# Performance work log

Hardware: AMD Instinct MI355X
Metric: run time of the kernel (lower is better)

Reference implementation:

```python
import jax, jax.numpy as jnp
import numpy as np

ENS, N_UNITS, N_HID, IN_DIM, OUT_DIM, BATCH = 10, 256, 7, 6, 201, 16384


def setup_inputs() -> dict:
    key = jax.random.key(0)
    ks = jax.random.split(key, 8)
    # He/fan-in scaled weights so activations stay sane through 8 ReLU layers
    W0 = jax.random.normal(ks[0], (ENS, IN_DIM, N_UNITS), jnp.float32) / np.sqrt(IN_DIM)
    b0 = jax.random.normal(ks[1], (ENS, N_UNITS), jnp.float32) * 0.01
    Wh = jax.random.normal(ks[2], (N_HID, ENS, N_UNITS, N_UNITS), jnp.float32) / np.sqrt(N_UNITS)
    bh = jax.random.normal(ks[3], (N_HID, ENS, N_UNITS), jnp.float32) * 0.01
    Wf = jax.random.normal(ks[4], (ENS, N_UNITS, OUT_DIM), jnp.float32) / np.sqrt(N_UNITS)
    bf = jax.random.normal(ks[5], (ENS, OUT_DIM), jnp.float32) * 0.01
    x = jax.random.normal(ks[6], (BATCH, IN_DIM), jnp.float32)
    return {"x": x, "W0": W0, "b0": b0, "Wh": Wh, "bh": bh, "Wf": Wf, "bf": bf}


def reference(x, W0, b0, Wh, bh, Wf, bf):
    # Ensemble of MLPs (grouped 1x1 conv == per-ensemble dense layers).
    # Input is broadcast to every ensemble member (torch.cat tiling).
    h = jax.nn.relu(jnp.einsum('bi,eio->beo', x, W0) + b0)  # (B, ens, 256)

    def step(h, wb):
        W, b = wb
        return jax.nn.relu(jnp.einsum('beh,eho->beo', h, W) + b), None

    h, _ = jax.lax.scan(step, h, (Wh, bh))  # 7 hidden layers
    y = jnp.einsum('beh,eho->beo', h, Wf) + bf  # (B, ens, out_dim), ens-major channels
    B, E, O = y.shape
    # Faithful to torch: view(B, out_dim, ens_size) on ens-major flat channels,
    # then mean over last dim (mixes strided channel chunks, not true ensemble mean).
    return y.reshape(B, O, E).mean(axis=-1)  # (B, out_dim)
```

## Files before the change

kernel.cpp:

```cpp
#include <hip/hip_runtime.h>

typedef unsigned int u32;
typedef unsigned short ushort_t;

typedef __attribute__((ext_vector_type(8)))  short bf16x8;
typedef __attribute__((ext_vector_type(16))) float f32x16;

#define ENS 10
#define NU 256
#define NHID 7
#define IN_DIM 6
#define OUT_DIM 201
#define BATCH 16384


#define WH_PER 65536
#define WH_TOT (NHID * ENS * WH_PER)
#define W0_PER 4096
#define W0_TOT (ENS * W0_PER)
#define WF_PER 57344
#define WF_TOT (ENS * WF_PER)
#define X_TOT ((BATCH / 32) * 64 * 8)

#define O_WHH 0
#define O_WHL (O_WHH + WH_TOT)
#define O_W0H (O_WHL + WH_TOT)
#define O_W0L (O_W0H + W0_TOT)
#define O_WFH (O_W0L + W0_TOT)
#define O_WFL (O_WFH + WF_TOT)
#define O_XH  (O_WFL + WF_TOT)
#define O_XL  (O_XH + X_TOT)
#define O_P   (O_XL + X_TOT)

#define NG 21
#define RS 264
#define YS 204
#define RT 64

__device__ __forceinline__ u32 bf16_rne(float f) {
    u32 u = __float_as_uint(f);
    return (u + 0x7FFFu + ((u >> 16) & 1u)) >> 16;
}
__device__ __forceinline__ void split2(float f, u32& h, u32& l) {
    h = bf16_rne(f);
    float fh = __uint_as_float(h << 16);
    l = bf16_rne(f - fh);
}

__device__ __forceinline__ u32 cvt_pk_bf16(float s0, float s1) {
    u32 r;
    asm("v_cvt_pk_bf16_f32 %0, %1, %2" : "=v"(r) : "v"(s0), "v"(s1));
    return r;
}


__global__ __launch_bounds__(256) void prep_wh(const float* __restrict__ Wh,
                                               ushort_t* __restrict__ dH, ushort_t* __restrict__ dL) {
    int i = blockIdx.x * 256 + threadIdx.x;
    if (i >= WH_TOT) return;
    int j = i & 7, l = (i >> 3) & 63, ctg = (i >> 9) & 7, s = (i >> 12) & 15, le = i >> 16;
    int k = s * 16 + ((l >> 5) << 3) + j;
    int n = ctg * 32 + (l & 31);
    float v = Wh[(size_t)le * 65536 + k * 256 + n];
    u32 h, lo; split2(v, h, lo);
    dH[i] = (ushort_t)h; dL[i] = (ushort_t)lo;
}

__global__ __launch_bounds__(256) void prep_w0(const float* __restrict__ W0,
                                               ushort_t* __restrict__ dH, ushort_t* __restrict__ dL) {
    int i = blockIdx.x * 256 + threadIdx.x;
    if (i >= W0_TOT) return;
    int j = i & 7, l = (i >> 3) & 63, ctg = (i >> 9) & 7, e = i >> 12;
    int k = ((l >> 5) << 3) + j;
    int n = ctg * 32 + (l & 31);
    float v = (k < IN_DIM) ? W0[(e * IN_DIM + k) * 256 + n] : 0.0f;
    u32 h, lo; split2(v, h, lo);
    dH[i] = (ushort_t)h; dL[i] = (ushort_t)lo;
}

__global__ __launch_bounds__(256) void prep_wf(const float* __restrict__ Wf,
                                               ushort_t* __restrict__ dH, ushort_t* __restrict__ dL) {
    int i = blockIdx.x * 256 + threadIdx.x;
    if (i >= WF_TOT) return;
    int e = i / WF_PER;
    int idx = i - e * WF_PER;
    int j = idx & 7, l = (idx >> 3) & 63, g = idx >> 9;
    int s = g / 7, ct = g - s * 7;
    int k = s * 16 + ((l >> 5) << 3) + j;
    int n = ct * 32 + (l & 31);
    float v = (n < OUT_DIM) ? Wf[((size_t)e * 256 + k) * OUT_DIM + n] : 0.0f;
    u32 h, lo; split2(v, h, lo);
    dH[i] = (ushort_t)h; dL[i] = (ushort_t)lo;
}

__global__ __launch_bounds__(256) void prep_x(const float* __restrict__ x,
                                              ushort_t* __restrict__ dH, ushort_t* __restrict__ dL) {
    int i = blockIdx.x * 256 + threadIdx.x;
    if (i >= X_TOT) return;
    int j = i & 7, l = (i >> 3) & 63, rt = i >> 9;
    int row = rt * 32 + (l & 31);
    int k = ((l >> 5) << 3) + j;
    float v = (k < IN_DIM) ? x[row * IN_DIM + k] : 0.0f;
    u32 h, lo; split2(v, h, lo);
    dH[i] = (ushort_t)h; dL[i] = (ushort_t)lo;
}

__global__ __launch_bounds__(256) void reduce_mean(const float* __restrict__ P,
                                                   float* __restrict__ out) {
    int i = blockIdx.x * 256 + threadIdx.x;
    if (i >= BATCH * OUT_DIM) return;
    int b = i / OUT_DIM, jo = i - b * OUT_DIM;
    int f0 = jo * 10;
    int e1 = f0 / OUT_DIM;
    int e2 = (f0 + 9) / OUT_DIM;
    int g1 = jo - (e1 * OUT_DIM) / 10;
    float s = P[((size_t)e1 * BATCH + b) * NG + g1];
    if (e2 != e1) {
        int g2 = jo - (e2 * OUT_DIM) / 10;
        s += P[((size_t)e2 * BATCH + b) * NG + g2];
    }
    out[i] = 0.1f * s;
}

#define MFMA32(A, B, C) __builtin_amdgcn_mfma_f32_32x32x16_bf16((A), (B), (C), 0, 0, 0)

__device__ __forceinline__ void store_act(ushort_t* actH, ushort_t* actL,
    const f32x16 (&acc)[2][2], float bv0, float bv1, int colA, int colB, int rowb)
{
#pragma unroll
    for (int mt = 0; mt < 2; ++mt)
#pragma unroll
        for (int c = 0; c < 2; ++c) {
            const float bv = c ? bv1 : bv0;
            const int col = c ? colB : colA;
#pragma unroll
            for (int q = 0; q < 4; ++q) {
#pragma unroll
                for (int p = 0; p < 2; ++p) {
                    int r0 = q * 4 + p * 2;
                    int row = mt * 32 + rowb + 8 * q + p * 2;
                    float g0 = fmaxf(acc[mt][c][r0] + bv, 0.0f);
                    float g1 = fmaxf(acc[mt][c][r0 + 1] + bv, 0.0f);
                    u32 hp = cvt_pk_bf16(g0, g1);
                    float fh0 = __uint_as_float(hp << 16);
                    float fh1 = __uint_as_float(hp & 0xFFFF0000u);
                    u32 lp = cvt_pk_bf16(g0 - fh0, g1 - fh1);
                    actH[row * RS + col]       = (ushort_t)hp;
                    actH[(row + 1) * RS + col] = (ushort_t)(hp >> 16);
                    actL[row * RS + col]       = (ushort_t)lp;
                    actL[(row + 1) * RS + col] = (ushort_t)(lp >> 16);
                }
            }
        }
}

__global__ __launch_bounds__(256, 2)
void mlp_mfma(const ushort_t* __restrict__ wsU,
              const float* __restrict__ b0g, const float* __restrict__ bhg,
              const float* __restrict__ bfg, float* __restrict__ Pws) {
    __shared__ __align__(16) ushort_t smem[2 * RT * RS];
    ushort_t* actH = smem;
    ushort_t* actL = smem + RT * RS;
    float*    yst  = (float*)smem;

    const int tid  = threadIdx.x;
    const int lane = tid & 63;
    const int cg   = tid >> 6;
    const int l31  = lane & 31;
    const int lh   = lane >> 5;
    const int ctg0 = cg * 2;

    const int bid  = blockIdx.x;
    const int work = (bid & 7) * 320 + (bid >> 3);
    const int e    = work >> 8;
    const int rb   = work & 255;
    const int rowWG = rb * RT;

    const size_t lo8 = (size_t)lane * 8;
    const ushort_t* arH0 = actH + l31 * RS;
    const ushort_t* arL0 = actL + l31 * RS;
    const ushort_t* arH1 = actH + (32 + l31) * RS;
    const ushort_t* arL1 = actL + (32 + l31) * RS;
    const int rowb = lh * 4;
    const int colA = ctg0 * 32 + l31, colB = colA + 32;

    f32x16 acc[2][2];
    bf16x8 Bc0, Bc1, Bc2, Bc3;
    bf16x8 aH[2], aL[2];

    {
        const ushort_t* B0H = wsU + O_W0H + (size_t)e * W0_PER;
        const ushort_t* B0L = wsU + O_W0L + (size_t)e * W0_PER;
        Bc0 = *(const bf16x8*)(B0H + (size_t)ctg0 * 512 + lo8);
        Bc1 = *(const bf16x8*)(B0L + (size_t)ctg0 * 512 + lo8);
        Bc2 = *(const bf16x8*)(B0H + (size_t)(ctg0 + 1) * 512 + lo8);
        Bc3 = *(const bf16x8*)(B0L + (size_t)(ctg0 + 1) * 512 + lo8);
#pragma unroll
        for (int mt = 0; mt < 2; ++mt) {
            size_t xoff = ((size_t)(rb * 2 + mt) * 64 + lane) * 8;
            aH[mt] = *(const bf16x8*)(wsU + O_XH + xoff);
            aL[mt] = *(const bf16x8*)(wsU + O_XL + xoff);
        }
        const ushort_t* BH0 = wsU + O_WHH + (size_t)e * WH_PER;
        const ushort_t* BL0 = wsU + O_WHL + (size_t)e * WH_PER;
        bf16x8 Bn0 = *(const bf16x8*)(BH0 + (size_t)ctg0 * 512 + lo8);
        bf16x8 Bn1 = *(const bf16x8*)(BL0 + (size_t)ctg0 * 512 + lo8);
        bf16x8 Bn2 = *(const bf16x8*)(BH0 + (size_t)(ctg0 + 1) * 512 + lo8);
        bf16x8 Bn3 = *(const bf16x8*)(BL0 + (size_t)(ctg0 + 1) * 512 + lo8);
        __builtin_amdgcn_sched_barrier(0);

        f32x16 z = 0.0f;
#pragma unroll
        for (int mt = 0; mt < 2; ++mt) {
            f32x16 a0 = z, a1 = z;
            a0 = MFMA32(aH[mt], Bc0, a0);
            a0 = MFMA32(aL[mt], Bc0, a0);
            a0 = MFMA32(aH[mt], Bc1, a0);
            a1 = MFMA32(aH[mt], Bc2, a1);
            a1 = MFMA32(aL[mt], Bc2, a1);
            a1 = MFMA32(aH[mt], Bc3, a1);
            acc[mt][0] = a0; acc[mt][1] = a1;
        }

        float bv0 = b0g[e * NU + colA];
        float bv1 = b0g[e * NU + colB];
        store_act(actH, actL, acc, bv0, bv1, colA, colB, rowb);
        Bc0 = Bn0; Bc1 = Bn1; Bc2 = Bn2; Bc3 = Bn3;
        __syncthreads();
    }

    const ushort_t* BH = wsU + O_WHH + (size_t)e * WH_PER;
    const ushort_t* BL = wsU + O_WHL + (size_t)e * WH_PER;
#pragma unroll 1
    for (int L = 0; L < NHID; ++L) {
        float bv0 = bhg[(size_t)(L * ENS + e) * NU + colA];
        float bv1 = bhg[(size_t)(L * ENS + e) * NU + colB];
        f32x16 z = 0.0f;
#pragma unroll
        for (int mt = 0; mt < 2; ++mt) { acc[mt][0] = z; acc[mt][1] = z; }
        aH[0] = *(const bf16x8*)(arH0 + lh * 8);
        aL[0] = *(const bf16x8*)(arL0 + lh * 8);
        aH[1] = *(const bf16x8*)(arH1 + lh * 8);
        aL[1] = *(const bf16x8*)(arL1 + lh * 8);

#pragma unroll
        for (int s = 0; s < 16; ++s) {
            bf16x8 aHn[2], aLn[2], Bn0, Bn1, Bn2, Bn3;
            if (s < 15) {
                int kn = (s + 1) * 16 + lh * 8;
                aHn[0] = *(const bf16x8*)(arH0 + kn);
                aLn[0] = *(const bf16x8*)(arL0 + kn);
                aHn[1] = *(const bf16x8*)(arH1 + kn);
                aLn[1] = *(const bf16x8*)(arL1 + kn);
                const ushort_t* ph = BH + (size_t)((s + 1) * 8 + ctg0) * 512;
                const ushort_t* pl = BL + (size_t)((s + 1) * 8 + ctg0) * 512;
                Bn0 = *(const bf16x8*)(ph + lo8);
                Bn1 = *(const bf16x8*)(pl + lo8);
                Bn2 = *(const bf16x8*)(ph + 512 + lo8);
                Bn3 = *(const bf16x8*)(pl + 512 + lo8);
            }
            __builtin_amdgcn_sched_barrier(0);
#pragma unroll
            for (int mt = 0; mt < 2; ++mt) {
                f32x16 a0 = acc[mt][0], a1 = acc[mt][1];
                a0 = MFMA32(aH[mt], Bc0, a0);
                a1 = MFMA32(aH[mt], Bc2, a1);
                a0 = MFMA32(aL[mt], Bc0, a0);
                a1 = MFMA32(aL[mt], Bc2, a1);
                a0 = MFMA32(aH[mt], Bc1, a0);
                a1 = MFMA32(aH[mt], Bc3, a1);
                acc[mt][0] = a0; acc[mt][1] = a1;
            }
            if (s < 15) {
                aH[0] = aHn[0]; aL[0] = aLn[0];
                aH[1] = aHn[1]; aL[1] = aLn[1];
                Bc0 = Bn0; Bc1 = Bn1; Bc2 = Bn2; Bc3 = Bn3;
            }
        }

        if (L < NHID - 1) {
            const ushort_t* nh = BH + (size_t)ENS * WH_PER;
            const ushort_t* nl = BL + (size_t)ENS * WH_PER;
            Bc0 = *(const bf16x8*)(nh + (size_t)ctg0 * 512 + lo8);
            Bc1 = *(const bf16x8*)(nl + (size_t)ctg0 * 512 + lo8);
            Bc2 = *(const bf16x8*)(nh + (size_t)(ctg0 + 1) * 512 + lo8);
            Bc3 = *(const bf16x8*)(nl + (size_t)(ctg0 + 1) * 512 + lo8);
        } else {
            const ushort_t* fh = wsU + O_WFH + (size_t)e * WF_PER;
            const ushort_t* fl = wsU + O_WFL + (size_t)e * WF_PER;
            int c0 = ctg0, c1 = (ctg0 + 1 > 6) ? 6 : ctg0 + 1;
            if (c0 > 6) c0 = 6;
            Bc0 = *(const bf16x8*)(fh + (size_t)c0 * 512 + lo8);
            Bc1 = *(const bf16x8*)(fl + (size_t)c0 * 512 + lo8);
            Bc2 = *(const bf16x8*)(fh + (size_t)c1 * 512 + lo8);
            Bc3 = *(const bf16x8*)(fl + (size_t)c1 * 512 + lo8);
        }

        __syncthreads();
        store_act(actH, actL, acc, bv0, bv1, colA, colB, rowb);
        __syncthreads();
        BH += (size_t)ENS * WH_PER;
        BL += (size_t)ENS * WH_PER;
    }

    {
        const ushort_t* FH = wsU + O_WFH + (size_t)e * WF_PER;
        const ushort_t* FL = wsU + O_WFL + (size_t)e * WF_PER;
        int c0 = (ctg0 > 6) ? 6 : ctg0;
        int c1 = (ctg0 + 1 > 6) ? 6 : ctg0 + 1;
        f32x16 z = 0.0f;
#pragma unroll
        for (int mt = 0; mt < 2; ++mt) { acc[mt][0] = z; acc[mt][1] = z; }
        aH[0] = *(const bf16x8*)(arH0 + lh * 8);
        aL[0] = *(const bf16x8*)(arL0 + lh * 8);
        aH[1] = *(const bf16x8*)(arH1 + lh * 8);
        aL[1] = *(const bf16x8*)(arL1 + lh * 8);

#pragma unroll
        for (int s = 0; s < 16; ++s) {
            bf16x8 aHn[2], aLn[2], Bn0, Bn1, Bn2, Bn3;
            if (s < 15) {
                int kn = (s + 1) * 16 + lh * 8;
                aHn[0] = *(const bf16x8*)(arH0 + kn);
                aLn[0] = *(const bf16x8*)(arL0 + kn);
                aHn[1] = *(const bf16x8*)(arH1 + kn);
                aLn[1] = *(const bf16x8*)(arL1 + kn);
                Bn0 = *(const bf16x8*)(FH + (size_t)((s + 1) * 7 + c0) * 512 + lo8);
                Bn1 = *(const bf16x8*)(FL + (size_t)((s + 1) * 7 + c0) * 512 + lo8);
                Bn2 = *(const bf16x8*)(FH + (size_t)((s + 1) * 7 + c1) * 512 + lo8);
                Bn3 = *(const bf16x8*)(FL + (size_t)((s + 1) * 7 + c1) * 512 + lo8);
            }
            __builtin_amdgcn_sched_barrier(0);
#pragma unroll
            for (int mt = 0; mt < 2; ++mt) {
                f32x16 a0 = acc[mt][0], a1 = acc[mt][1];
                a0 = MFMA32(aH[mt], Bc0, a0);
                a1 = MFMA32(aH[mt], Bc2, a1);
                a0 = MFMA32(aL[mt], Bc0, a0);
                a1 = MFMA32(aL[mt], Bc2, a1);
                a0 = MFMA32(aH[mt], Bc1, a0);
                a1 = MFMA32(aH[mt], Bc3, a1);
                acc[mt][0] = a0; acc[mt][1] = a1;
            }
            if (s < 15) {
                aH[0] = aHn[0]; aL[0] = aLn[0];
                aH[1] = aHn[1]; aL[1] = aLn[1];
                Bc0 = Bn0; Bc1 = Bn1; Bc2 = Bn2; Bc3 = Bn3;
            }
        }

        int o0 = ctg0 * 32 + l31;
        int o1 = (ctg0 + 1) * 32 + l31;
        bool v0 = (o0 < OUT_DIM);
        bool v1 = (ctg0 + 1 < 7) && (o1 < OUT_DIM);
        float bf0 = v0 ? bfg[e * OUT_DIM + o0] : 0.0f;
        float bf1 = v1 ? bfg[e * OUT_DIM + o1] : 0.0f;

        __syncthreads();
#pragma unroll
        for (int mt = 0; mt < 2; ++mt)
#pragma unroll
            for (int r = 0; r < 16; ++r) {
                int row = mt * 32 + rowb + (r & 3) + 8 * (r >> 2);
                if (v0) yst[row * YS + o0] = acc[mt][0][r] + bf0;
                if (v1) yst[row * YS + o1] = acc[mt][1][r] + bf1;
            }
        __syncthreads();

        const int base_jo = (e * OUT_DIM) / 10;
        const int e201 = e * OUT_DIM;
        for (int it = tid; it < RT * NG; it += 256) {
            int row = it / NG;
            int g   = it - row * NG;
            int f0  = (base_jo + g) * 10;
            float sm = 0.0f;
#pragma unroll
            for (int d = 0; d < 10; ++d) {
                int oo = f0 + d - e201;
                if (oo >= 0 && oo < OUT_DIM) sm += yst[row * YS + oo];
            }
            Pws[((size_t)e * BATCH + rowWG + row) * NG + g] = sm;
        }
    }
}

extern "C" void kernel_launch(void* const* d_in, const int* in_sizes, int n_in,
                              void* d_out, int out_size, void* d_ws, size_t ws_size,
                              hipStream_t stream) {
    const float* x  = (const float*)d_in[0];
    const float* W0 = (const float*)d_in[1];
    const float* b0 = (const float*)d_in[2];
    const float* Wh = (const float*)d_in[3];
    const float* bh = (const float*)d_in[4];
    const float* Wf = (const float*)d_in[5];
    const float* bf = (const float*)d_in[6];
    float* out = (float*)d_out;
    ushort_t* ws = (ushort_t*)d_ws;
    float* Pws = (float*)(ws + O_P);

    prep_wh<<<(WH_TOT + 255) / 256, 256, 0, stream>>>(Wh, ws + O_WHH, ws + O_WHL);
    prep_w0<<<(W0_TOT + 255) / 256, 256, 0, stream>>>(W0, ws + O_W0H, ws + O_W0L);
    prep_wf<<<(WF_TOT + 255) / 256, 256, 0, stream>>>(Wf, ws + O_WFH, ws + O_WFL);
    prep_x <<<(X_TOT  + 255) / 256, 256, 0, stream>>>(x,  ws + O_XH,  ws + O_XL);

    mlp_mfma<<<dim3(BATCH / RT * ENS), 256, 0, stream>>>(ws, b0, bh, bf, Pws);
    reduce_mean<<<(BATCH * OUT_DIM + 255) / 256, 256, 0, stream>>>(Pws, out);
}
```

Baseline: 440.0 us.

## Prefetch weight fragments two k-steps ahead with inline asm loads and waitcnt

Replaces the one-step-ahead weight register prefetch with a four-slot ring of inline-asm global_load_dwordx4 that fetches B fragments two k-steps ahead, waiting with explicit s_waitcnt vmcnt(4). The next layer's first two fragments are issued during the current layer's last steps, so global-load latency is hidden across layer boundaries. It also reorders the first-layer MFMAs and hoists the bias loads. In exchange it uses more VGPRs for the ring and relies on manual vmcnt accounting, which can break if the compiler interleaves other vector-memory ops.

```diff
diff --git a/kernel.cpp b/kernel.cpp
--- a/kernel.cpp
+++ b/kernel.cpp
@@ -52,6 +52,11 @@
     asm("v_cvt_pk_bf16_f32 %0, %1, %2" : "=v"(r) : "v"(s0), "v"(s1));
     return r;
 }
+
+#define GLOAD(dst, p) \
+    asm volatile("global_load_dwordx4 %0, %1, off" : "=v"(dst) : "v"(p))
+#define VMWAIT4 asm volatile("s_waitcnt vmcnt(4)" ::: "memory")
+#define VMWAIT0 asm volatile("s_waitcnt vmcnt(0)" ::: "memory")
 
 
 __global__ __launch_bounds__(256) void prep_wh(const float* __restrict__ Wh,
@@ -184,48 +189,57 @@
     const int rowb = lh * 4;
     const int colA = ctg0 * 32 + l31, colB = colA + 32;
 
+    const int c0f = (ctg0 > 6) ? 6 : ctg0;
+    const int c1f = (ctg0 + 1 > 6) ? 6 : ctg0 + 1;
+
     f32x16 acc[2][2];
-    bf16x8 Bc0, Bc1, Bc2, Bc3;
     bf16x8 aH[2], aL[2];
+    bf16x8 sB0h[4], sB0l[4], sB1h[4], sB1l[4];
 
     {
         const ushort_t* B0H = wsU + O_W0H + (size_t)e * W0_PER;
         const ushort_t* B0L = wsU + O_W0L + (size_t)e * W0_PER;
-        Bc0 = *(const bf16x8*)(B0H + (size_t)ctg0 * 512 + lo8);
-        Bc1 = *(const bf16x8*)(B0L + (size_t)ctg0 * 512 + lo8);
-        Bc2 = *(const bf16x8*)(B0H + (size_t)(ctg0 + 1) * 512 + lo8);
-        Bc3 = *(const bf16x8*)(B0L + (size_t)(ctg0 + 1) * 512 + lo8);
+        bf16x8 b0h0 = *(const bf16x8*)(B0H + (size_t)ctg0 * 512 + lo8);
+        bf16x8 b0l0 = *(const bf16x8*)(B0L + (size_t)ctg0 * 512 + lo8);
+        bf16x8 b0h1 = *(const bf16x8*)(B0H + (size_t)(ctg0 + 1) * 512 + lo8);
+        bf16x8 b0l1 = *(const bf16x8*)(B0L + (size_t)(ctg0 + 1) * 512 + lo8);
+        bf16x8 xh[2], xl[2];
 #pragma unroll
         for (int mt = 0; mt < 2; ++mt) {
             size_t xoff = ((size_t)(rb * 2 + mt) * 64 + lane) * 8;
-            aH[mt] = *(const bf16x8*)(wsU + O_XH + xoff);
-            aL[mt] = *(const bf16x8*)(wsU + O_XL + xoff);
-        }
-        const ushort_t* BH0 = wsU + O_WHH + (size_t)e * WH_PER;
-        const ushort_t* BL0 = wsU + O_WHL + (size_t)e * WH_PER;
-        bf16x8 Bn0 = *(const bf16x8*)(BH0 + (size_t)ctg0 * 512 + lo8);
-        bf16x8 Bn1 = *(const bf16x8*)(BL0 + (size_t)ctg0 * 512 + lo8);
-        bf16x8 Bn2 = *(const bf16x8*)(BH0 + (size_t)(ctg0 + 1) * 512 + lo8);
-        bf16x8 Bn3 = *(const bf16x8*)(BL0 + (size_t)(ctg0 + 1) * 512 + lo8);
-        __builtin_amdgcn_sched_barrier(0);
+            xh[mt] = *(const bf16x8*)(wsU + O_XH + xoff);
+            xl[mt] = *(const bf16x8*)(wsU + O_XL + xoff);
+        }
+        float bv0 = b0g[e * NU + colA];
+        float bv1 = b0g[e * NU + colB];
 
         f32x16 z = 0.0f;
 #pragma unroll
         for (int mt = 0; mt < 2; ++mt) {
             f32x16 a0 = z, a1 = z;
-            a0 = MFMA32(aH[mt], Bc0, a0);
-            a0 = MFMA32(aL[mt], Bc0, a0);
-            a0 = MFMA32(aH[mt], Bc1, a0);
-            a1 = MFMA32(aH[mt], Bc2, a1);
-            a1 = MFMA32(aL[mt], Bc2, a1);
-            a1 = MFMA32(aH[mt], Bc3, a1);
+            a0 = MFMA32(xh[mt], b0h0, a0);
+            a1 = MFMA32(xh[mt], b0h1, a1);
+            a0 = MFMA32(xl[mt], b0h0, a0);
+            a1 = MFMA32(xl[mt], b0h1, a1);
+            a0 = MFMA32(xh[mt], b0l0, a0);
+            a1 = MFMA32(xh[mt], b0l1, a1);
             acc[mt][0] = a0; acc[mt][1] = a1;
         }
 
-        float bv0 = b0g[e * NU + colA];
-        float bv1 = b0g[e * NU + colB];
+        VMWAIT0;
+        {
+            const ushort_t* BH0 = wsU + O_WHH + (size_t)e * WH_PER;
+            const ushort_t* BL0 = wsU + O_WHL + (size_t)e * WH_PER;
+#pragma unroll
+            for (int cc = 0; cc < 2; ++cc) {
+                size_t off = ((size_t)(cc * 8 + ctg0)) * 512 + lo8;
+                GLOAD(sB0h[cc], BH0 + off);
+                GLOAD(sB0l[cc], BL0 + off);
+                GLOAD(sB1h[cc], BH0 + off + 512);
+                GLOAD(sB1l[cc], BL0 + off + 512);
+            }
+        }
         store_act(actH, actL, acc, bv0, bv1, colA, colB, rowb);
-        Bc0 = Bn0; Bc1 = Bn1; Bc2 = Bn2; Bc3 = Bn3;
         __syncthreads();
     }
 
@@ -235,6 +249,29 @@
     for (int L = 0; L < NHID; ++L) {
         float bv0 = bhg[(size_t)(L * ENS + e) * NU + colA];
         float bv1 = bhg[(size_t)(L * ENS + e) * NU + colB];
+
+        const ushort_t *nA0[2], *nB0[2], *nA1[2], *nB1[2];
+        if (L < NHID - 1) {
+            const ushort_t* a_ = BH + (size_t)ENS * WH_PER;
+            const ushort_t* b_ = BL + (size_t)ENS * WH_PER;
+#pragma unroll
+            for (int cc = 0; cc < 2; ++cc) {
+                size_t off = ((size_t)(cc * 8 + ctg0)) * 512 + lo8;
+                nA0[cc] = a_ + off;       nB0[cc] = b_ + off;
+                nA1[cc] = a_ + off + 512; nB1[cc] = b_ + off + 512;
+            }
+        } else {
+            const ushort_t* fh = wsU + O_WFH + (size_t)e * WF_PER;
+            const ushort_t* fl = wsU + O_WFL + (size_t)e * WF_PER;
+#pragma unroll
+            for (int cc = 0; cc < 2; ++cc) {
+                size_t o0_ = ((size_t)(cc * 7 + c0f)) * 512 + lo8;
+                size_t o1_ = ((size_t)(cc * 7 + c1f)) * 512 + lo8;
+                nA0[cc] = fh + o0_; nB0[cc] = fl + o0_;
+                nA1[cc] = fh + o1_; nB1[cc] = fl + o1_;
+            }
+        }
+
         f32x16 z = 0.0f;
 #pragma unroll
         for (int mt = 0; mt < 2; ++mt) { acc[mt][0] = z; acc[mt][1] = z; }
@@ -243,57 +280,50 @@
         aH[1] = *(const bf16x8*)(arH1 + lh * 8);
         aL[1] = *(const bf16x8*)(arL1 + lh * 8);
 
+        VMWAIT0;
+
 #pragma unroll
         for (int s = 0; s < 16; ++s) {
-            bf16x8 aHn[2], aLn[2], Bn0, Bn1, Bn2, Bn3;
+            bf16x8 aHn[2], aLn[2];
             if (s < 15) {
                 int kn = (s + 1) * 16 + lh * 8;
                 aHn[0] = *(const bf16x8*)(arH0 + kn);
                 aLn[0] = *(const bf16x8*)(arL0 + kn);
                 aHn[1] = *(const bf16x8*)(arH1 + kn);
                 aLn[1] = *(const bf16x8*)(arL1 + kn);
-                const ushort_t* ph = BH + (size_t)((s + 1) * 8 + ctg0) * 512;
-                const ushort_t* pl = BL + (size_t)((s + 1) * 8 + ctg0) * 512;
-                Bn0 = *(const bf16x8*)(ph + lo8);
-                Bn1 = *(const bf16x8*)(pl + lo8);
-                Bn2 = *(const bf16x8*)(ph + 512 + lo8);
-                Bn3 = *(const bf16x8*)(pl + 512 + lo8);
-            }
+            }
+            {
+                const ushort_t *pA0, *pB0, *pA1, *pB1;
+                if (s < 14) {
+                    size_t off = ((size_t)((s + 2) * 8 + ctg0)) * 512 + lo8;
+                    pA0 = BH + off; pB0 = BL + off;
+                    pA1 = BH + off + 512; pB1 = BL + off + 512;
+                } else {
+                    pA0 = nA0[s - 14]; pB0 = nB0[s - 14];
+                    pA1 = nA1[s - 14]; pB1 = nB1[s - 14];
+                }
+                GLOAD(sB0h[(s + 2) & 3], pA0);
+                GLOAD(sB0l[(s + 2) & 3], pB0);
+                GLOAD(sB1h[(s + 2) & 3], pA1);
+                GLOAD(sB1l[(s + 2) & 3], pB1);
+            }
+            VMWAIT4;
             __builtin_amdgcn_sched_barrier(0);
 #pragma unroll
             for (int mt = 0; mt < 2; ++mt) {
                 f32x16 a0 = acc[mt][0], a1 = acc[mt][1];
-                a0 = MFMA32(aH[mt], Bc0, a0);
-                a1 = MFMA32(aH[mt], Bc2, a1);
-                a0 = MFMA32(aL[mt], Bc0, a0);
-                a1 = MFMA32(aL[mt], Bc2, a1);
-                a0 = MFMA32(aH[mt], Bc1, a0);
-                a1 = MFMA32(aH[mt], Bc3, a1);
+                a0 = MFMA32(aH[mt], sB0h[s & 3], a0);
+                a1 = MFMA32(aH[mt], sB1h[s & 3], a1);
+                a0 = MFMA32(aL[mt], sB0h[s & 3], a0);
+                a1 = MFMA32(aL[mt], sB1h[s & 3], a1);
+                a0 = MFMA32(aH[mt], sB0l[s & 3], a0);
+                a1 = MFMA32(aH[mt], sB1l[s & 3], a1);
                 acc[mt][0] = a0; acc[mt][1] = a1;
             }
             if (s < 15) {
                 aH[0] = aHn[0]; aL[0] = aLn[0];
                 aH[1] = aHn[1]; aL[1] = aLn[1];
-                Bc0 = Bn0; Bc1 = Bn1; Bc2 = Bn2; Bc3 = Bn3;
-            }
-        }
-
-        if (L < NHID - 1) {
-            const ushort_t* nh = BH + (size_t)ENS * WH_PER;
-            const ushort_t* nl = BL + (size_t)ENS * WH_PER;
-            Bc0 = *(const bf16x8*)(nh + (size_t)ctg0 * 512 + lo8);
-            Bc1 = *(const bf16x8*)(nl + (size_t)ctg0 * 512 + lo8);
-            Bc2 = *(const bf16x8*)(nh + (size_t)(ctg0 + 1) * 512 + lo8);
-            Bc3 = *(const bf16x8*)(nl + (size_t)(ctg0 + 1) * 512 + lo8);
-        } else {
-            const ushort_t* fh = wsU + O_WFH + (size_t)e * WF_PER;
-            const ushort_t* fl = wsU + O_WFL + (size_t)e * WF_PER;
-            int c0 = ctg0, c1 = (ctg0 + 1 > 6) ? 6 : ctg0 + 1;
-            if (c0 > 6) c0 = 6;
-            Bc0 = *(const bf16x8*)(fh + (size_t)c0 * 512 + lo8);
-            Bc1 = *(const bf16x8*)(fl + (size_t)c0 * 512 + lo8);
-            Bc2 = *(const bf16x8*)(fh + (size_t)c1 * 512 + lo8);
-            Bc3 = *(const bf16x8*)(fl + (size_t)c1 * 512 + lo8);
+            }
         }
 
         __syncthreads();
@@ -306,8 +336,13 @@
     {
         const ushort_t* FH = wsU + O_WFH + (size_t)e * WF_PER;
         const ushort_t* FL = wsU + O_WFL + (size_t)e * WF_PER;
-        int c0 = (ctg0 > 6) ? 6 : ctg0;
-        int c1 = (ctg0 + 1 > 6) ? 6 : ctg0 + 1;
+        int o0 = ctg0 * 32 + l31;
+        int o1 = (ctg0 + 1) * 32 + l31;
+        bool v0 = (o0 < OUT_DIM);
+        bool v1 = (ctg0 + 1 < 7) && (o1 < OUT_DIM);
+        float bf0 = v0 ? bfg[e * OUT_DIM + o0] : 0.0f;
+        float bf1 = v1 ? bfg[e * OUT_DIM + o1] : 0.0f;
+
         f32x16 z = 0.0f;
 #pragma unroll
         for (int mt = 0; mt < 2; ++mt) { acc[mt][0] = z; acc[mt][1] = z; }
@@ -316,45 +351,44 @@
         aH[1] = *(const bf16x8*)(arH1 + lh * 8);
         aL[1] = *(const bf16x8*)(arL1 + lh * 8);
 
+        VMWAIT0;
+
 #pragma unroll
         for (int s = 0; s < 16; ++s) {
-            bf16x8 aHn[2], aLn[2], Bn0, Bn1, Bn2, Bn3;
+            bf16x8 aHn[2], aLn[2];
             if (s < 15) {
                 int kn = (s + 1) * 16 + lh * 8;
                 aHn[0] = *(const bf16x8*)(arH0 + kn);
                 aLn[0] = *(const bf16x8*)(arL0 + kn);
                 aHn[1] = *(const bf16x8*)(arH1 + kn);
                 aLn[1] = *(const bf16x8*)(arL1 + kn);
-                Bn0 = *(const bf16x8*)(FH + (size_t)((s + 1) * 7 + c0) * 512 + lo8);
-                Bn1 = *(const bf16x8*)(FL + (size_t)((s + 1) * 7 + c0) * 512 + lo8);
-                Bn2 = *(const bf16x8*)(FH + (size_t)((s + 1) * 7 + c1) * 512 + lo8);
-                Bn3 = *(const bf16x8*)(FL + (size_t)((s + 1) * 7 + c1) * 512 + lo8);
-            }
+            }
+            if (s < 14) {
+                size_t o0_ = ((size_t)((s + 2) * 7 + c0f)) * 512 + lo8;
+                size_t o1_ = ((size_t)((s + 2) * 7 + c1f)) * 512 + lo8;
+                GLOAD(sB0h[(s + 2) & 3], FH + o0_);
+                GLOAD(sB0l[(s + 2) & 3], FL + o0_);
+                GLOAD(sB1h[(s + 2) & 3], FH + o1_);
+                GLOAD(sB1l[(s + 2) & 3], FL + o1_);
+            }
+            if (s < 15) { VMWAIT4; } else { VMWAIT0; }
             __builtin_amdgcn_sched_barrier(0);
 #pragma unroll
             for (int mt = 0; mt < 2; ++mt) {
                 f32x16 a0 = acc[mt][0], a1 = acc[mt][1];
-                a0 = MFMA32(aH[mt], Bc0, a0);
-                a1 = MFMA32(aH[mt], Bc2, a1);
-                a0 = MFMA32(aL[mt], Bc0, a0);
-                a1 = MFMA32(aL[mt], Bc2, a1);
-                a0 = MFMA32(aH[mt], Bc1, a0);
-                a1 = MFMA32(aH[mt], Bc3, a1);
+                a0 = MFMA32(aH[mt], sB0h[s & 3], a0);
+                a1 = MFMA32(aH[mt], sB1h[s & 3], a1);
+                a0 = MFMA32(aL[mt], sB0h[s & 3], a0);
+                a1 = MFMA32(aL[mt], sB1h[s & 3], a1);
+                a0 = MFMA32(aH[mt], sB0l[s & 3], a0);
+                a1 = MFMA32(aH[mt], sB1l[s & 3], a1);
                 acc[mt][0] = a0; acc[mt][1] = a1;
             }
             if (s < 15) {
                 aH[0] = aHn[0]; aL[0] = aLn[0];
                 aH[1] = aHn[1]; aL[1] = aLn[1];
-                Bc0 = Bn0; Bc1 = Bn1; Bc2 = Bn2; Bc3 = Bn3;
-            }
-        }
-
-        int o0 = ctg0 * 32 + l31;
-        int o1 = (ctg0 + 1) * 32 + l31;
-        bool v0 = (o0 < OUT_DIM);
-        bool v1 = (ctg0 + 1 < 7) && (o1 < OUT_DIM);
-        float bf0 = v0 ? bfg[e * OUT_DIM + o0] : 0.0f;
-        float bf1 = v1 ? bfg[e * OUT_DIM + o1] : 0.0f;
+            }
+        }
 
         __syncthreads();
 #pragma unroll
```

After: 428.7 us. -2.6%, faster.
